# Performance work log

Measured on AMD Instinct MI355X. Metric: run time of the kernel, lower is better.

## Reference

```python
import jax, jax.numpy as jnp
import numpy as np

ALPHA = 1.0   # get_spike_fn('ArcTan', 1.0, 20.0)
WIDTH = 20.0

@jax.custom_vjp
def arctan_spike(x):
    # Heaviside forward, ArcTan surrogate gradient
    return (x > 0).astype(x.dtype)

def _spike_fwd(x):
    return arctan_spike(x), x

def _spike_bwd(x, g):
    return (g * ALPHA / (1.0 + (WIDTH * x) ** 2),)

arctan_spike.defvjp(_spike_fwd, _spike_bwd)

T, B, F = 2048, 64, 512  # seq_len, batch, features (input_groups=256 -> F=512)
TAU_SYN, TAU_MEM, V_THRESH, W_SCALE = 0.08, 0.03, 1.0, 0.4

def setup_inputs() -> dict:
    key = jax.random.key(0)
    x = jax.random.normal(key, (T, B, F), dtype=jnp.float32)
    # ff weight: block_diag of input_groups copies of 0.4*I2 == 0.4*I_F
    W = (W_SCALE * jnp.eye(F, dtype=jnp.float32))
    leak_i = jnp.full((F,), 1.0 - TAU_SYN, dtype=jnp.float32)
    leak_v = jnp.full((F,), 1.0 - TAU_MEM, dtype=jnp.float32)
    thresh = jnp.full((F,), V_THRESH, dtype=jnp.float32)
    return {"x": x, "W": W, "leak_i": leak_i, "leak_v": leak_v, "thresh": thresh}

def reference(x, W, leak_i, leak_v, thresh):
    Tn, Bn, Fn = x.shape
    i0 = jnp.zeros((Bn, Fn), dtype=x.dtype)
    v0 = jnp.zeros((Bn, Fn), dtype=x.dtype)
    z0 = jnp.zeros((Bn, Fn), dtype=x.dtype)

    def step(carry, xt):
        i, v, z = carry
        ff = xt @ W.T                      # [B,F] linear synapse (no bias)
        i_new = leak_i * i + ff            # leaky synaptic current
        v_new = leak_v * v * (1.0 - z) + i_new  # membrane, reset-to-zero on spike
        z_new = arctan_spike(v_new - thresh)
        return (i_new, v_new, z_new), z_new

    _, out = jax.lax.scan(step, (i0, v0, z0), x)
    return out  # [T, B, F]
```

## Files before the change

kernel.cpp:

```cpp
#include <hip/hip_runtime.h>


typedef float v2f __attribute__((ext_vector_type(2)));

constexpr int T_STEPS = 2048;
constexpr int B_DIM   = 64;
constexpr int F_DIM   = 512;
constexpr int BF      = B_DIM * F_DIM;
constexpr int NPAIR   = BF / 2;
constexpr int CHUNK   = 16;
constexpr int NCHUNK  = T_STEPS / CHUNK;

__global__ __launch_bounds__(64, 2) void snn_scan_kernel(
    const float* __restrict__ x,
    const float* __restrict__ W,
    const float* __restrict__ leak_i,
    const float* __restrict__ leak_v,
    const float* __restrict__ thresh,
    float* __restrict__ out) {

    const int p  = blockIdx.x * 64 + threadIdx.x;
    const int e  = 2 * p;
    const int f0 = e & (F_DIM - 1);

    const float w00 = W[(size_t)(f0    ) * F_DIM + f0    ];
    const float w01 = W[(size_t)(f0    ) * F_DIM + f0 + 1];
    const float w10 = W[(size_t)(f0 + 1) * F_DIM + f0    ];
    const float w11 = W[(size_t)(f0 + 1) * F_DIM + f0 + 1];
    const float li0 = leak_i[f0], li1 = leak_i[f0 + 1];
    const float lv0 = leak_v[f0], lv1 = leak_v[f0 + 1];
    const float th0 = thresh[f0], th1 = thresh[f0 + 1];

    float i0 = 0.0f, v0 = 0.0f, z0 = 0.0f;
    float i1 = 0.0f, v1 = 0.0f, z1 = 0.0f;

    const v2f* xp = (const v2f*)(x + e);
    v2f*       op = (v2f*)(out + e);

    v2f bufA[CHUNK], bufB[CHUNK], bufC[CHUNK], bufD[CHUNK];

    auto load_chunk = [&](int c, v2f (&buf)[CHUNK]) {
        const v2f* ptr = xp + (size_t)c * (CHUNK * NPAIR);
        #pragma unroll
        for (int j = 0; j < CHUNK; ++j)
            buf[j] = __builtin_nontemporal_load(ptr + (size_t)j * NPAIR);
    };

    auto process_chunk = [&](int c, v2f (&buf)[CHUNK]) {
        v2f* o = op + (size_t)c * (CHUNK * NPAIR);
        #pragma unroll
        for (int j = 0; j < CHUNK; ++j) {
            const float xe = buf[j].x;
            const float xo = buf[j].y;
            const float ff0 = __fadd_rn(__fmul_rn(w00, xe), __fmul_rn(w01, xo));
            const float ff1 = __fadd_rn(__fmul_rn(w10, xe), __fmul_rn(w11, xo));
            i0 = __fadd_rn(__fmul_rn(li0, i0), ff0);
            i1 = __fadd_rn(__fmul_rn(li1, i1), ff1);
            float vm0 = __fmul_rn(lv0, v0);
            float vm1 = __fmul_rn(lv1, v1);
            vm0 = (z0 > 0.0f) ? 0.0f : vm0;
            vm1 = (z1 > 0.0f) ? 0.0f : vm1;
            v0 = __fadd_rn(vm0, i0);
            v1 = __fadd_rn(vm1, i1);
            z0 = (v0 > th0) ? 1.0f : 0.0f;
            z1 = (v1 > th1) ? 1.0f : 0.0f;
            v2f zv; zv.x = z0; zv.y = z1;
            __builtin_nontemporal_store(zv, o + (size_t)j * NPAIR);
        }
    };

    load_chunk(0, bufA);
    load_chunk(1, bufB);
    load_chunk(2, bufC);
    for (int c = 0; c < NCHUNK; c += 4) {
        if (c + 3 < NCHUNK) load_chunk(c + 3, bufD);
        process_chunk(c, bufA);
        if (c + 4 < NCHUNK) load_chunk(c + 4, bufA);
        process_chunk(c + 1, bufB);
        if (c + 5 < NCHUNK) load_chunk(c + 5, bufB);
        process_chunk(c + 2, bufC);
        if (c + 6 < NCHUNK) load_chunk(c + 6, bufC);
        process_chunk(c + 3, bufD);
    }
}

extern "C" void kernel_launch(void* const* d_in, const int* in_sizes, int n_in,
                              void* d_out, int out_size, void* d_ws, size_t ws_size,
                              hipStream_t stream) {
    const float* x      = (const float*)d_in[0];
    const float* W      = (const float*)d_in[1];
    const float* leak_i = (const float*)d_in[2];
    const float* leak_v = (const float*)d_in[3];
    const float* thresh = (const float*)d_in[4];
    float* out = (float*)d_out;

    snn_scan_kernel<<<dim3(NPAIR / 64), dim3(64), 0, stream>>>(
        x, W, leak_i, leak_v, thresh, out);
}
```

Measured before the change: 438.1 us.

## Warp-specialize producer waves staging x chunks into double-buffered LDS

Splits each block into four producer waves that load 64-step chunks of x into double-buffered LDS with 16-byte loads, and one consumer wave that runs the serial recurrence from LDS and writes spikes. The aim is to take global-load latency off the serial dependency chain and use wider, better-coalesced loads. In exchange it adds a block barrier per chunk, and because only one wave per block computes, concurrency depends on how many blocks fit per CU given the 64KB of LDS each.

Result: faster. 425.5 us (-2.9%).

```diff
diff --git a/kernel.cpp b/kernel.cpp
--- a/kernel.cpp
+++ b/kernel.cpp
@@ -2,16 +2,22 @@
 
 
 typedef float v2f __attribute__((ext_vector_type(2)));
+typedef float v4f __attribute__((ext_vector_type(4)));
 
 constexpr int T_STEPS = 2048;
 constexpr int B_DIM   = 64;
 constexpr int F_DIM   = 512;
 constexpr int BF      = B_DIM * F_DIM;
-constexpr int NPAIR   = BF / 2;
-constexpr int CHUNK   = 16;
+constexpr int BLK_FLOATS = 128;
+constexpr int NBLK    = BF / BLK_FLOATS;
+constexpr int CHUNK   = 64;
 constexpr int NCHUNK  = T_STEPS / CHUNK;
+constexpr int NPROD   = 4;
+constexpr int STEPS_PER_PROD = CHUNK / NPROD;
+constexpr int LOADS_PER_PROD = STEPS_PER_PROD / 2;
+constexpr int LDS_FLOATS = 2 * CHUNK * BLK_FLOATS;
 
-__global__ __launch_bounds__(64, 2) void snn_scan_kernel(
+__global__ __launch_bounds__(320, 1) void snn_scan_kernel(
     const float* __restrict__ x,
     const float* __restrict__ W,
     const float* __restrict__ leak_i,
@@ -19,39 +25,60 @@
     const float* __restrict__ thresh,
     float* __restrict__ out) {
 
-    const int p  = blockIdx.x * 64 + threadIdx.x;
-    const int e  = 2 * p;
+    __shared__ float lds[LDS_FLOATS];
+
+    const int tid  = threadIdx.x;
+    const int wid  = tid >> 6;
+    const int lane = tid & 63;
+    const int blk  = blockIdx.x;
+    const bool is_prod = (wid < NPROD);
+
+    const int  half = lane >> 5;
+    const int  l32  = lane & 31;
+    const int  sbase = wid * STEPS_PER_PROD + half;
+    const float* xsrc = x + (size_t)blk * BLK_FLOATS + (size_t)l32 * 4;
+
+    const int e  = blk * BLK_FLOATS + lane * 2;
     const int f0 = e & (F_DIM - 1);
+    float w00 = 0.f, w01 = 0.f, w10 = 0.f, w11 = 0.f;
+    float li0 = 0.f, li1 = 0.f, lv0 = 0.f, lv1 = 0.f, th0 = 0.f, th1 = 0.f;
+    if (!is_prod) {
+        w00 = W[(size_t)(f0    ) * F_DIM + f0    ];
+        w01 = W[(size_t)(f0    ) * F_DIM + f0 + 1];
+        w10 = W[(size_t)(f0 + 1) * F_DIM + f0    ];
+        w11 = W[(size_t)(f0 + 1) * F_DIM + f0 + 1];
+        li0 = leak_i[f0]; li1 = leak_i[f0 + 1];
+        lv0 = leak_v[f0]; lv1 = leak_v[f0 + 1];
+        th0 = thresh[f0]; th1 = thresh[f0 + 1];
+    }
+    float i0 = 0.f, v0 = 0.f, z0 = 0.f;
+    float i1 = 0.f, v1 = 0.f, z1 = 0.f;
+    float* osrc = out + e;
 
-    const float w00 = W[(size_t)(f0    ) * F_DIM + f0    ];
-    const float w01 = W[(size_t)(f0    ) * F_DIM + f0 + 1];
-    const float w10 = W[(size_t)(f0 + 1) * F_DIM + f0    ];
-    const float w11 = W[(size_t)(f0 + 1) * F_DIM + f0 + 1];
-    const float li0 = leak_i[f0], li1 = leak_i[f0 + 1];
-    const float lv0 = leak_v[f0], lv1 = leak_v[f0 + 1];
-    const float th0 = thresh[f0], th1 = thresh[f0 + 1];
-
-    float i0 = 0.0f, v0 = 0.0f, z0 = 0.0f;
-    float i1 = 0.0f, v1 = 0.0f, z1 = 0.0f;
-
-    const v2f* xp = (const v2f*)(x + e);
-    v2f*       op = (v2f*)(out + e);
-
-    v2f bufA[CHUNK], bufB[CHUNK], bufC[CHUNK], bufD[CHUNK];
-
-    auto load_chunk = [&](int c, v2f (&buf)[CHUNK]) {
-        const v2f* ptr = xp + (size_t)c * (CHUNK * NPAIR);
+    auto produce = [&](int c) {
+        const int db = c & 1;
+        const float* gb = xsrc + (size_t)(c * CHUNK + sbase) * BF;
+        v4f r[LOADS_PER_PROD];
         #pragma unroll
-        for (int j = 0; j < CHUNK; ++j)
-            buf[j] = __builtin_nontemporal_load(ptr + (size_t)j * NPAIR);
+        for (int i = 0; i < LOADS_PER_PROD; ++i)
+            r[i] = __builtin_nontemporal_load(
+                       (const v4f*)(gb + (size_t)(2 * i) * BF));
+        float* lb = &lds[(size_t)db * (CHUNK * BLK_FLOATS)
+                         + (size_t)sbase * BLK_FLOATS + (size_t)l32 * 4];
+        #pragma unroll
+        for (int i = 0; i < LOADS_PER_PROD; ++i)
+            *(v4f*)(lb + (size_t)(2 * i) * BLK_FLOATS) = r[i];
     };
 
-    auto process_chunk = [&](int c, v2f (&buf)[CHUNK]) {
-        v2f* o = op + (size_t)c * (CHUNK * NPAIR);
-        #pragma unroll
+    auto consume = [&](int c) {
+        const int db = c & 1;
+        const float* lb = &lds[(size_t)db * (CHUNK * BLK_FLOATS) + (size_t)lane * 2];
+        float* ob = osrc + (size_t)c * CHUNK * BF;
+        #pragma unroll 8
         for (int j = 0; j < CHUNK; ++j) {
-            const float xe = buf[j].x;
-            const float xo = buf[j].y;
+            const v2f xv = *(const v2f*)(lb + (size_t)j * BLK_FLOATS);
+            const float xe = xv.x;
+            const float xo = xv.y;
             const float ff0 = __fadd_rn(__fmul_rn(w00, xe), __fmul_rn(w01, xo));
             const float ff1 = __fadd_rn(__fmul_rn(w10, xe), __fmul_rn(w11, xo));
             i0 = __fadd_rn(__fmul_rn(li0, i0), ff0);
@@ -65,22 +92,20 @@
             z0 = (v0 > th0) ? 1.0f : 0.0f;
             z1 = (v1 > th1) ? 1.0f : 0.0f;
             v2f zv; zv.x = z0; zv.y = z1;
-            __builtin_nontemporal_store(zv, o + (size_t)j * NPAIR);
+            __builtin_nontemporal_store(zv, (v2f*)(ob + (size_t)j * BF));
         }
     };
 
-    load_chunk(0, bufA);
-    load_chunk(1, bufB);
-    load_chunk(2, bufC);
-    for (int c = 0; c < NCHUNK; c += 4) {
-        if (c + 3 < NCHUNK) load_chunk(c + 3, bufD);
-        process_chunk(c, bufA);
-        if (c + 4 < NCHUNK) load_chunk(c + 4, bufA);
-        process_chunk(c + 1, bufB);
-        if (c + 5 < NCHUNK) load_chunk(c + 5, bufB);
-        process_chunk(c + 2, bufC);
-        if (c + 6 < NCHUNK) load_chunk(c + 6, bufC);
-        process_chunk(c + 3, bufD);
+    if (is_prod) produce(0);
+    __syncthreads();
+
+    for (int c = 0; c < NCHUNK; ++c) {
+        if (is_prod) {
+            if (c + 1 < NCHUNK) produce(c + 1);
+        } else {
+            consume(c);
+        }
+        __syncthreads();
     }
 }
 
@@ -94,6 +119,6 @@
     const float* thresh = (const float*)d_in[4];
     float* out = (float*)d_out;
 
-    snn_scan_kernel<<<dim3(NPAIR / 64), dim3(64), 0, stream>>>(
+    snn_scan_kernel<<<dim3(NBLK), dim3(320), 0, stream>>>(
         x, W, leak_i, leak_v, thresh, out);
 }
```
